# Performance work log

Measured on AMD Instinct MI355X. Metric: run time of the kernel, lower is better.

The kernel has to match this reference:

```python
import jax, jax.numpy as jnp
import numpy as np
from jax import lax

B, T, C = 32, 512, 128
K = 3                      # top_k periods
MIN_P, MAX_P = 8, 64       # period search band
P_MAX = MAX_P              # grid width
CYC_MAX = (T + MIN_P - 1) // MIN_P
KW = 9                     # cyc-axis depthwise kernel
GN_G = 32                  # _best_gn_groups(128)
EPS_GN = 1e-5
EPS_ORTH = 1e-6
EPS_W = 1e-8


def setup_inputs() -> dict:
    key = jax.random.key(0)
    ks = jax.random.split(key, 4)
    return {
        "x": jax.random.normal(ks[0], (B, T, C), jnp.float32),
        "W_dw": jax.random.normal(ks[1], (C, 1, KW), jnp.float32) * 0.1,
        "W_pw": jax.random.normal(ks[2], (C, C), jnp.float32) * (1.0 / np.sqrt(C)),
        "gn_weight": jnp.ones((C,), jnp.float32),
        "gn_bias": jnp.zeros((C,), jnp.float32),
        "W_gate": jax.random.normal(ks[3], (C, C), jnp.float32) * (1.0 / np.sqrt(C)),
        "gamma": jnp.full((C,), 1e-3, jnp.float32),
    }


def _autocorr_topk(x):
    # x: [B,T,C] -> period idx [B,K], softmax weights [B,K]
    Xf = jnp.fft.rfft(x, axis=1)
    Pm = (Xf * jnp.conj(Xf)).real.mean(-1)          # [B, T//2+1]
    r = jnp.fft.irfft(Pm, n=T, axis=1)              # [B, T] autocorrelation
    lag = jnp.arange(T)
    valid = (lag >= MIN_P) & (lag <= MAX_P)
    very_neg = jnp.finfo(x.dtype).min / 8
    rm = jnp.where(valid[None, :], r, very_neg)
    vals, idx = lax.top_k(rm, K)
    w = jax.nn.softmax(vals, axis=1)
    return idx, w


def _fold(s, p):
    # s: [N,T,C], p: [N] int periods -> Z [N,C,CYC_MAX,P_MAX], mask, unfold index maps
    N = s.shape[0]
    p = jnp.maximum(p, 1)
    tpad = ((T + p - 1) // p) * p                   # [N]
    cyc = jnp.arange(CYC_MAX)[None, :, None]
    pos = jnp.arange(P_MAX)[None, None, :]
    time = cyc * p[:, None, None] + pos             # [N,CYC_MAX,P_MAX]
    valid = (pos < p[:, None, None]) & (time < tpad[:, None, None])
    # right-side reflect padding indices
    m = 2 * (T - 1)
    rr = time % m
    src_idx = jnp.where(rr < T, rr, m - rr)
    src = jnp.take_along_axis(s, src_idx.reshape(N, -1)[:, :, None], axis=1)
    src = src.reshape(N, CYC_MAX, P_MAX, C) * valid[..., None].astype(s.dtype)
    Z = jnp.transpose(src, (0, 3, 1, 2))            # [N,C,CYC_MAX,P_MAX]
    mask2d = valid[:, None].astype(s.dtype)         # [N,1,CYC_MAX,P_MAX]
    t = jnp.arange(T)[None, :]
    cyc_T = jnp.clip(t // p[:, None], 0, CYC_MAX - 1)
    pos_T = jnp.clip(t % p[:, None], 0, P_MAX - 1)
    return Z, mask2d, cyc_T, pos_T


def _cyc_conv(Z, mask2d, W_dw, W_pw, gn_w, gn_b, W_gate, gamma):
    # CycAxisConv1d: mean over period axis, depthwise+pointwise conv along cyc,
    # GroupNorm, GELU, SE-gate, LayerScale residual broadcast back to 2D.
    N, _, L, _ = Z.shape
    u = Z.mean(-1)                                  # [N,C,L]
    h = lax.conv_general_dilated(u, W_dw, (1,), [(KW // 2, KW // 2)],
                                 dimension_numbers=('NCH', 'OIH', 'NCH'),
                                 feature_group_count=C)
    h = jnp.einsum('oc,ncl->nol', W_pw, h)
    hg = h.reshape(N, GN_G, C // GN_G, L)
    mean = hg.mean((2, 3), keepdims=True)
    var = hg.var((2, 3), keepdims=True)
    hg = (hg - mean) * lax.rsqrt(var + EPS_GN)
    h = hg.reshape(N, C, L) * gn_w[None, :, None] + gn_b[None, :, None]
    h = jax.nn.gelu(h, approximate=False)
    gate = jax.nn.sigmoid(jnp.einsum('oc,nc->no', W_gate, u.mean(-1)))
    h = h * gate[:, :, None]
    x2d = h[..., None] * gamma[None, :, None, None] * mask2d
    return Z + x2d


def _unfold(Z, cyc_T, pos_T):
    N = Z.shape[0]
    Zf = Z.reshape(N, C, CYC_MAX * P_MAX)
    sp = jnp.clip(cyc_T * P_MAX + pos_T, 0, CYC_MAX * P_MAX - 1)  # [N,T]
    y = jnp.take_along_axis(Zf, sp[:, None, :], axis=2)           # [N,C,T]
    return jnp.transpose(y, (0, 2, 1))                            # [N,T,C]


def reference(x, W_dw, W_pw, gn_weight, gn_bias, W_gate, gamma):
    idx, w = _autocorr_topk(x)                      # [B,K], [B,K]
    p_flat = idx.reshape(-1)                        # [B*K]
    s = jnp.repeat(x, K, axis=0)                    # [B*K,T,C]
    Z, mask2d, cyc_T, pos_T = _fold(s, p_flat)
    Z = _cyc_conv(Z, mask2d, W_dw, W_pw, gn_weight, gn_bias, W_gate, gamma)
    y = _unfold(Z, cyc_T, pos_T).reshape(B, K, T, C)
    periodic = jnp.einsum('bk,bktc->btc', w, y)
    # period confidence Gamma from weight entropy
    H = -(w * jnp.log(w + EPS_W)).sum(1)
    Gamma = jnp.clip(1.0 - H / (jnp.log(float(K) + EPS_W) + EPS_W), 0.0, 1.0)
    # orthogonal residual of local part against periodic part
    local = x - periodic
    num = (local * periodic).sum(1, keepdims=True)
    den = (periodic * periodic).sum(1, keepdims=True) + EPS_ORTH
    local_orth = local - num / den * periodic
    g = Gamma[:, None, None]
    return g * (periodic + local_orth) + (1.0 - g) * x
```

## Files before the change

### kernel.cpp

```cpp
#include <hip/hip_runtime.h>
#include <math.h>

static constexpr int Bn   = 32;
static constexpr int Tn   = 512;
static constexpr int Cn   = 128;
static constexpr int NLAG = 57;
static constexpr int CYC  = 64;

__global__ __launch_bounds__(256) void k_autocorr(const float* __restrict__ x,
    float* __restrict__ r_ws) {
  const int w   = (blockIdx.x & 7) * 32 + (blockIdx.x >> 3);
  const int b   = w >> 3;
  const int grp = w & 7;
  const int L0  = 8 + grp * 8;
  const int tid = threadIdx.x;
  const float4* X4 = (const float4*)(x + (size_t)b * Tn * Cn);

  float acc[8];
#pragma unroll
  for (int i = 0; i < 8; ++i) acc[i] = 0.f;

  for (int it = 0; it < 8; ++it) {
    const int id = it * 256 + tid;
    const int c4 = id & 31;
    const int t0 = (id >> 5) * 8;
    float4 A[8];
#pragma unroll
    for (int j = 0; j < 8; ++j) A[j] = X4[(t0 + j) * 32 + c4];
    float4 R[16];
#pragma unroll
    for (int j = 0; j < 16; ++j) R[j] = X4[((t0 + L0 + j) & 511) * 32 + c4];
#pragma unroll
    for (int g = 0; g < 8; ++g) {
#pragma unroll
      for (int j = 0; j < 8; ++j) {
        const float4 a = A[j];
        const float4 r = R[g + j];
        acc[g] += a.x * r.x + a.y * r.y + a.z * r.z + a.w * r.w;
      }
    }
  }

  __shared__ float lds_r[4][8];
  const int lane = tid & 63, wave = tid >> 6;
#pragma unroll
  for (int g = 0; g < 8; ++g) {
    float v = acc[g];
#pragma unroll
    for (int m = 32; m > 0; m >>= 1) v += __shfl_xor(v, m, 64);
    if (lane == 0) lds_r[wave][g] = v;
  }
  __syncthreads();
  if (tid < 8) {
    const int li = grp * 8 + tid;
    if (li < NLAG) {
      r_ws[b * NLAG + li] =
          (lds_r[0][tid] + lds_r[1][tid] + lds_r[2][tid] + lds_r[3][tid]) * (1.0f / Cn);
    }
  }
}

__global__ __launch_bounds__(512) void k_fold_conv(
    const float* __restrict__ x, const float* __restrict__ r_ws,
    const float* __restrict__ Wdw, const float* __restrict__ Wpw,
    const float* __restrict__ gnw, const float* __restrict__ gnb,
    const float* __restrict__ Wgate, float* __restrict__ hh) {
  const int n  = (blockIdx.x & 7) * 12 + (blockIdx.x >> 3);
  const int b  = n / 3, kk = n % 3;
  const int tid  = threadIdx.x;
  const int lane = tid & 63;
  const int wq   = __builtin_amdgcn_readfirstlane(tid >> 6);

  __shared__ float su[CYC * 129];
  __shared__ float sh[Cn * 65];
  __shared__ float ubar_s[Cn];
  __shared__ float gates_s[Cn];
  __shared__ int   p_sh;

  if (tid < 64) {
    const float* rb = r_ws + b * NLAG;
    float v  = (tid < NLAG) ? rb[tid] : -INFINITY;
    int  idx = tid;
    int  lag = 8;
#pragma unroll
    for (int k = 0; k < 3; ++k) {
      if (k > kk) break;
      float bv = v; int bi = idx;
#pragma unroll
      for (int m = 32; m > 0; m >>= 1) {
        const float ov = __shfl_xor(bv, m, 64);
        const int   oi = __shfl_xor(bi, m, 64);
        if (ov > bv || (ov == bv && oi < bi)) { bv = ov; bi = oi; }
      }
      lag = bi + 8;
      if (idx == bi) v = -INFINITY;
    }
    if (tid == 0) p_sh = lag;
  }
  __syncthreads();
  const int p    = p_sh;
  const int ncyc = (Tn + p - 1) / p;

  {
    const int l  = tid >> 3;
    const int c0 = (tid & 7) * 16;
    float a[16];
#pragma unroll
    for (int i = 0; i < 16; ++i) a[i] = 0.f;
    if (l < ncyc) {
      const float4* xb4 = (const float4*)(x + (size_t)b * Tn * Cn) + (c0 >> 2);
      const int base = l * p;
      for (int j = 0; j < p; ++j) {
        const int time = base + j;
        const int src  = time < Tn ? time : (2 * (Tn - 1) - time);
        const float4 v0 = xb4[src * 32 + 0];
        const float4 v1 = xb4[src * 32 + 1];
        const float4 v2 = xb4[src * 32 + 2];
        const float4 v3 = xb4[src * 32 + 3];
        a[0]  += v0.x; a[1]  += v0.y; a[2]  += v0.z; a[3]  += v0.w;
        a[4]  += v1.x; a[5]  += v1.y; a[6]  += v1.z; a[7]  += v1.w;
        a[8]  += v2.x; a[9]  += v2.y; a[10] += v2.z; a[11] += v2.w;
        a[12] += v3.x; a[13] += v3.y; a[14] += v3.z; a[15] += v3.w;
      }
    }
    float* dst = su + l * 129 + c0;
#pragma unroll
    for (int i = 0; i < 16; ++i) dst[i] = a[i] * (1.0f / 64.0f);
  }
  __syncthreads();

  if (tid < Cn) {
    float s = 0.f;
    for (int l = 0; l < CYC; ++l) s += su[l * 129 + tid];
    ubar_s[tid] = s * (1.0f / CYC);
  }

  {
    const int c0 = wq * 16;
#pragma unroll
    for (int i = 0; i < 16; ++i) {
      const int c = c0 + i;
      float s = 0.f;
#pragma unroll
      for (int k = 0; k < 9; ++k) {
        const int ll = lane + k - 4;
        if (ll >= 0 && ll < CYC) s += su[ll * 129 + c] * Wdw[c * 9 + k];
      }
      sh[c * 65 + lane] = s;
    }
  }
  __syncthreads();

  {
    const int ol   = lane & 15;
    const int part = lane >> 4;
    const int o    = wq * 16 + ol;
    float z = 0.f;
    const float* wg = Wgate + (size_t)o * Cn + part * 32;
    const float* ub = ubar_s + part * 32;
    for (int c = 0; c < 32; ++c) z += wg[c] * ub[c];
    z += __shfl_xor(z, 16, 64);
    z += __shfl_xor(z, 32, 64);
    if (part == 0) gates_s[o] = 1.0f / (1.0f + expf(-z));
  }

  float acc[16];
#pragma unroll
  for (int i = 0; i < 16; ++i) acc[i] = 0.f;
  const int o0 = wq * 16;
  {
    const float* wb = Wpw + (size_t)o0 * Cn;
    for (int c = 0; c < Cn; ++c) {
      const float hv = sh[c * 65 + lane];
#pragma unroll
      for (int i = 0; i < 16; ++i) acc[i] = fmaf(wb[i * Cn + c], hv, acc[i]);
    }
  }
  __syncthreads();

  float4 res[4];
#pragma unroll
  for (int g = 0; g < 4; ++g) {
    float s1 = acc[4*g] + acc[4*g+1] + acc[4*g+2] + acc[4*g+3];
    float s2 = acc[4*g]*acc[4*g] + acc[4*g+1]*acc[4*g+1]
             + acc[4*g+2]*acc[4*g+2] + acc[4*g+3]*acc[4*g+3];
#pragma unroll
    for (int m = 32; m > 0; m >>= 1) {
      s1 += __shfl_xor(s1, m, 64);
      s2 += __shfl_xor(s2, m, 64);
    }
    const float mean = s1 * (1.0f / 256.0f);
    const float var  = s2 * (1.0f / 256.0f) - mean * mean;
    const float rstd = rsqrtf(var + 1e-5f);
    float* rp = (float*)&res[g];
#pragma unroll
    for (int i = 0; i < 4; ++i) {
      const int o = o0 + 4*g + i;
      float h = (acc[4*g + i] - mean) * rstd;
      h = h * gnw[o] + gnb[o];
      h = 0.5f * h * (1.0f + erff(h * 0.70710678118654752440f));
      rp[i] = h * gates_s[o];
    }
  }
  float4* hp = (float4*)(hh + (size_t)n * CYC * Cn + (size_t)lane * Cn + o0);
#pragma unroll
  for (int g = 0; g < 4; ++g) hp[g] = res[g];
}

__global__ __launch_bounds__(128) void k_dot_out(
    const float* __restrict__ x, const float* __restrict__ hh,
    const float* __restrict__ r_ws, const float* __restrict__ gamma,
    float* __restrict__ out) {
  const int b  = blockIdx.x;
  const int cg = blockIdx.y;
  const int tid = threadIdx.x;
  const int c_l = tid & 15;
  const int tg  = tid >> 4;
  const int c   = cg * 16 + c_l;

  __shared__ float P_s[Tn * 16];
  __shared__ unsigned short cyc_s[Tn][3];
  __shared__ float params[4];
  __shared__ int   pp[3];
  __shared__ float red[2][2][16];
  __shared__ float sc_s[16];

  if (tid < 64) {
    const float* rb = r_ws + b * NLAG;
    float v  = (tid < NLAG) ? rb[tid] : -INFINITY;
    int  idx = tid;
    float vals[3]; int lags[3];
#pragma unroll
    for (int k = 0; k < 3; ++k) {
      float bv = v; int bi = idx;
#pragma unroll
      for (int m = 32; m > 0; m >>= 1) {
        const float ov = __shfl_xor(bv, m, 64);
        const int   oi = __shfl_xor(bi, m, 64);
        if (ov > bv || (ov == bv && oi < bi)) { bv = ov; bi = oi; }
      }
      vals[k] = bv; lags[k] = bi + 8;
      if (idx == bi) v = -INFINITY;
    }
    if (tid == 0) {
      const float m  = vals[0];
      const float e0 = expf(vals[0] - m), e1 = expf(vals[1] - m), e2 = expf(vals[2] - m);
      const float s  = e0 + e1 + e2;
      const float w0 = e0 / s, w1 = e1 / s, w2 = e2 / s;
      pp[0] = lags[0]; pp[1] = lags[1]; pp[2] = lags[2];
      params[0] = w0; params[1] = w1; params[2] = w2;
      const float H  = -(w0 * logf(w0 + 1e-8f) + w1 * logf(w1 + 1e-8f) + w2 * logf(w2 + 1e-8f));
      const float lg = logf(3.0f + 1e-8f) + 1e-8f;
      params[3] = fminf(fmaxf(1.0f - H / lg, 0.0f), 1.0f);
    }
  }
  __syncthreads();
  const int p0 = pp[0], p1 = pp[1], p2 = pp[2];
  const float w0 = params[0], w1 = params[1], w2 = params[2];
  const float g  = params[3];
  const float sw = w0 + w1 + w2;

  for (int t = tid; t < Tn; t += 128) {
    cyc_s[t][0] = (unsigned short)(t / p0);
    cyc_s[t][1] = (unsigned short)(t / p1);
    cyc_s[t][2] = (unsigned short)(t / p2);
  }
  __syncthreads();

  const float gam = gamma[c];
  const float* xb = x + (size_t)b * Tn * Cn;
  const float* h0 = hh + (size_t)(b * 3 + 0) * CYC * Cn + c;
  const float* h1 = hh + (size_t)(b * 3 + 1) * CYC * Cn + c;
  const float* h2 = hh + (size_t)(b * 3 + 2) * CYC * Cn + c;

  float na = 0.f, da = 0.f;
  for (int tt = 0; tt < 64; ++tt) {
    const int t = (tg << 6) + tt;
    const float xv = xb[t * Cn + c];
    const float dv = gam * (w0 * h0[cyc_s[t][0] * Cn] +
                            w1 * h1[cyc_s[t][1] * Cn] +
                            w2 * h2[cyc_s[t][2] * Cn]);
    const float P = sw * xv + dv;
    P_s[t * 16 + c_l] = P;
    na += (xv - P) * P;
    da += P * P;
  }
  na += __shfl_xor(na, 16, 64); da += __shfl_xor(da, 16, 64);
  na += __shfl_xor(na, 32, 64); da += __shfl_xor(da, 32, 64);
  const int wv_ = tid >> 6;
  if ((tid & 63) < 16) { red[0][wv_][c_l] = na; red[1][wv_][c_l] = da; }
  __syncthreads();
  if (tid < 16) {
    const float num = red[0][0][tid] + red[0][1][tid];
    const float den = red[1][0][tid] + red[1][1][tid] + 1e-6f;
    sc_s[tid] = g * (num / den);
  }
  __syncthreads();
  const float sc = sc_s[c_l];

  float* ob = out + (size_t)b * Tn * Cn;
  for (int tt = 0; tt < 64; ++tt) {
    const int t = (tg << 6) + tt;
    const float xv = xb[t * Cn + c];
    ob[t * Cn + c] = xv - sc * P_s[t * 16 + c_l];
  }
}

extern "C" void kernel_launch(void* const* d_in, const int* in_sizes, int n_in,
                              void* d_out, int out_size, void* d_ws, size_t ws_size,
                              hipStream_t stream) {
  const float* x     = (const float*)d_in[0];
  const float* Wdw   = (const float*)d_in[1];
  const float* Wpw   = (const float*)d_in[2];
  const float* gnw   = (const float*)d_in[3];
  const float* gnb   = (const float*)d_in[4];
  const float* Wgate = (const float*)d_in[5];
  const float* gamma = (const float*)d_in[6];
  float* out = (float*)d_out;

  char* ws = (char*)d_ws;
  float* r_ws = (float*)ws;
  float* hh   = (float*)(ws + 8192);

  k_autocorr<<<Bn * 8, 256, 0, stream>>>(x, r_ws);
  k_fold_conv<<<Bn * 3, 512, 0, stream>>>(x, r_ws, Wdw, Wpw, gnw, gnb, Wgate, hh);
  k_dot_out<<<dim3(Bn, 8), 128, 0, stream>>>(x, hh, r_ws, gamma, out);
}
```

Measured before the change: 150.7 us.

## Split fold and conv into separate kernels with finer-grained parallel grids

The single 96-block fold+conv kernel becomes two kernels. A 6144-block fold kernel computes per-cycle sums into a workspace buffer, and a 768-block conv kernel splits the output channels into 8 groups per sequence, with the gate computed per wave through shuffles. The output kernel moves to 256-thread blocks on a 1D remapped grid with interleaved time indexing. The aim is to fill the GPU's compute units instead of running 96 large blocks. The cost is an extra launch, a workspace round-trip, and the depthwise conv plus gate being recomputed in each of the 8 channel-group blocks.

```diff
diff --git a/kernel.cpp b/kernel.cpp
--- a/kernel.cpp
+++ b/kernel.cpp
@@ -6,6 +6,27 @@
 static constexpr int Cn   = 128;
 static constexpr int NLAG = 57;
 static constexpr int CYC  = 64;
+
+__device__ __forceinline__ int topk_p(const float* __restrict__ rb,
+                                      int tid, int kk) {
+  float v  = (tid < NLAG) ? rb[tid] : -INFINITY;
+  int  idx = tid;
+  int  lag = 8;
+#pragma unroll
+  for (int k = 0; k < 3; ++k) {
+    if (k > kk) break;
+    float bv = v; int bi = idx;
+#pragma unroll
+    for (int m = 32; m > 0; m >>= 1) {
+      const float ov = __shfl_xor(bv, m, 64);
+      const int   oi = __shfl_xor(bi, m, 64);
+      if (ov > bv || (ov == bv && oi < bi)) { bv = ov; bi = oi; }
+    }
+    lag = bi + 8;
+    if (idx == bi) v = -INFINITY;
+  }
+  return lag;
+}
 
 __global__ __launch_bounds__(256) void k_autocorr(const float* __restrict__ x,
     float* __restrict__ r_ws) {
@@ -60,159 +81,156 @@
   }
 }
 
-__global__ __launch_bounds__(512) void k_fold_conv(
-    const float* __restrict__ x, const float* __restrict__ r_ws,
-    const float* __restrict__ Wdw, const float* __restrict__ Wpw,
-    const float* __restrict__ gnw, const float* __restrict__ gnb,
-    const float* __restrict__ Wgate, float* __restrict__ hh) {
-  const int n  = (blockIdx.x & 7) * 12 + (blockIdx.x >> 3);
-  const int b  = n / 3, kk = n % 3;
-  const int tid  = threadIdx.x;
-  const int lane = tid & 63;
-  const int wq   = __builtin_amdgcn_readfirstlane(tid >> 6);
-
-  __shared__ float su[CYC * 129];
-  __shared__ float sh[Cn * 65];
-  __shared__ float ubar_s[Cn];
-  __shared__ float gates_s[Cn];
-  __shared__ int   p_sh;
-
+__global__ __launch_bounds__(128) void k_fold_u(const float* __restrict__ x,
+    const float* __restrict__ r_ws, float* __restrict__ u) {
+  const int bid = blockIdx.x;
+  const int w = (bid & 7) * 768 + (bid >> 3);
+  const int n = w >> 6, l = w & 63;
+  const int b = n / 3, kk = n % 3;
+  const int tid = threadIdx.x;
+
+  __shared__ int p_sh;
   if (tid < 64) {
-    const float* rb = r_ws + b * NLAG;
-    float v  = (tid < NLAG) ? rb[tid] : -INFINITY;
-    int  idx = tid;
-    int  lag = 8;
-#pragma unroll
-    for (int k = 0; k < 3; ++k) {
-      if (k > kk) break;
-      float bv = v; int bi = idx;
-#pragma unroll
-      for (int m = 32; m > 0; m >>= 1) {
-        const float ov = __shfl_xor(bv, m, 64);
-        const int   oi = __shfl_xor(bi, m, 64);
-        if (ov > bv || (ov == bv && oi < bi)) { bv = ov; bi = oi; }
-      }
-      lag = bi + 8;
-      if (idx == bi) v = -INFINITY;
-    }
+    const int lag = topk_p(r_ws + b * NLAG, tid, kk);
     if (tid == 0) p_sh = lag;
   }
   __syncthreads();
   const int p    = p_sh;
   const int ncyc = (Tn + p - 1) / p;
 
+  float acc = 0.f;
+  if (l < ncyc) {
+    const float* xb = x + (size_t)b * Tn * Cn;
+    const int base = l * p;
+    for (int j = 0; j < p; ++j) {
+      const int time = base + j;
+      const int src  = time < Tn ? time : (2 * (Tn - 1) - time);
+      acc += xb[src * Cn + tid];
+    }
+  }
+  u[((size_t)n * CYC + l) * Cn + tid] = acc * (1.0f / 64.0f);
+}
+
+__global__ __launch_bounds__(256) void k_conv(
+    const float* __restrict__ u, const float* __restrict__ Wdw,
+    const float* __restrict__ Wpw, const float* __restrict__ gnw,
+    const float* __restrict__ gnb, const float* __restrict__ Wgate,
+    float* __restrict__ hh) {
+  const int bid = blockIdx.x;
+  const int w = (bid & 7) * 96 + (bid >> 3);
+  const int n = w >> 3, og = w & 7;
+  const int tid  = threadIdx.x;
+  const int l    = tid & 63;
+  const int wq   = __builtin_amdgcn_readfirstlane(tid >> 6);
+
+  __shared__ float smem[8320];
+  __shared__ float ubar_s[Cn];
+
   {
-    const int l  = tid >> 3;
-    const int c0 = (tid & 7) * 16;
-    float a[16];
-#pragma unroll
-    for (int i = 0; i < 16; ++i) a[i] = 0.f;
-    if (l < ncyc) {
-      const float4* xb4 = (const float4*)(x + (size_t)b * Tn * Cn) + (c0 >> 2);
-      const int base = l * p;
-      for (int j = 0; j < p; ++j) {
-        const int time = base + j;
-        const int src  = time < Tn ? time : (2 * (Tn - 1) - time);
-        const float4 v0 = xb4[src * 32 + 0];
-        const float4 v1 = xb4[src * 32 + 1];
-        const float4 v2 = xb4[src * 32 + 2];
-        const float4 v3 = xb4[src * 32 + 3];
-        a[0]  += v0.x; a[1]  += v0.y; a[2]  += v0.z; a[3]  += v0.w;
-        a[4]  += v1.x; a[5]  += v1.y; a[6]  += v1.z; a[7]  += v1.w;
-        a[8]  += v2.x; a[9]  += v2.y; a[10] += v2.z; a[11] += v2.w;
-        a[12] += v3.x; a[13] += v3.y; a[14] += v3.z; a[15] += v3.w;
-      }
-    }
-    float* dst = su + l * 129 + c0;
-#pragma unroll
-    for (int i = 0; i < 16; ++i) dst[i] = a[i] * (1.0f / 64.0f);
+    const float4* u4 = (const float4*)(u + (size_t)n * CYC * Cn);
+#pragma unroll
+    for (int i = 0; i < 8; ++i) {
+      const int idx4 = i * 256 + tid;
+      const float4 v = u4[idx4];
+      const int ll = idx4 >> 5;
+      const int cc = (idx4 & 31) << 2;
+      float* d = smem + ll * 129 + cc;
+      d[0] = v.x; d[1] = v.y; d[2] = v.z; d[3] = v.w;
+    }
   }
   __syncthreads();
 
   if (tid < Cn) {
     float s = 0.f;
-    for (int l = 0; l < CYC; ++l) s += su[l * 129 + tid];
+    for (int ll = 0; ll < CYC; ++ll) s += smem[ll * 129 + tid];
     ubar_s[tid] = s * (1.0f / CYC);
   }
 
+  float hreg[32];
   {
-    const int c0 = wq * 16;
-#pragma unroll
-    for (int i = 0; i < 16; ++i) {
+    const int c0 = wq * 32;
+#pragma unroll
+    for (int i = 0; i < 32; ++i) {
       const int c = c0 + i;
       float s = 0.f;
 #pragma unroll
       for (int k = 0; k < 9; ++k) {
-        const int ll = lane + k - 4;
-        if (ll >= 0 && ll < CYC) s += su[ll * 129 + c] * Wdw[c * 9 + k];
+        const int ll = l + k - 4;
+        if (ll >= 0 && ll < CYC) s += smem[ll * 129 + c] * Wdw[c * 9 + k];
       }
-      sh[c * 65 + lane] = s;
-    }
-  }
-  __syncthreads();
-
+      hreg[i] = s;
+    }
+  }
+  __syncthreads();
+
+  float gi[4];
   {
-    const int ol   = lane & 15;
-    const int part = lane >> 4;
-    const int o    = wq * 16 + ol;
+    const int ol   = l & 3;
+    const int part = l >> 2;
+    const int o    = og * 16 + wq * 4 + ol;
     float z = 0.f;
-    const float* wg = Wgate + (size_t)o * Cn + part * 32;
-    const float* ub = ubar_s + part * 32;
-    for (int c = 0; c < 32; ++c) z += wg[c] * ub[c];
+    const float* wg = Wgate + (size_t)o * Cn + part * 8;
+    const float* ub = ubar_s + part * 8;
+#pragma unroll
+    for (int cc = 0; cc < 8; ++cc) z += wg[cc] * ub[cc];
+    z += __shfl_xor(z, 4, 64);
+    z += __shfl_xor(z, 8, 64);
     z += __shfl_xor(z, 16, 64);
     z += __shfl_xor(z, 32, 64);
-    if (part == 0) gates_s[o] = 1.0f / (1.0f + expf(-z));
-  }
-
-  float acc[16];
-#pragma unroll
-  for (int i = 0; i < 16; ++i) acc[i] = 0.f;
-  const int o0 = wq * 16;
+    const float sig = 1.0f / (1.0f + expf(-z));
+#pragma unroll
+    for (int i = 0; i < 4; ++i) gi[i] = __shfl(sig, i, 64);
+  }
+
   {
-    const float* wb = Wpw + (size_t)o0 * Cn;
-    for (int c = 0; c < Cn; ++c) {
-      const float hv = sh[c * 65 + lane];
-#pragma unroll
-      for (int i = 0; i < 16; ++i) acc[i] = fmaf(wb[i * Cn + c], hv, acc[i]);
-    }
-  }
-  __syncthreads();
-
-  float4 res[4];
-#pragma unroll
-  for (int g = 0; g < 4; ++g) {
-    float s1 = acc[4*g] + acc[4*g+1] + acc[4*g+2] + acc[4*g+3];
-    float s2 = acc[4*g]*acc[4*g] + acc[4*g+1]*acc[4*g+1]
-             + acc[4*g+2]*acc[4*g+2] + acc[4*g+3]*acc[4*g+3];
-#pragma unroll
-    for (int m = 32; m > 0; m >>= 1) {
-      s1 += __shfl_xor(s1, m, 64);
-      s2 += __shfl_xor(s2, m, 64);
-    }
-    const float mean = s1 * (1.0f / 256.0f);
-    const float var  = s2 * (1.0f / 256.0f) - mean * mean;
-    const float rstd = rsqrtf(var + 1e-5f);
-    float* rp = (float*)&res[g];
-#pragma unroll
-    for (int i = 0; i < 4; ++i) {
-      const int o = o0 + 4*g + i;
-      float h = (acc[4*g + i] - mean) * rstd;
-      h = h * gnw[o] + gnb[o];
-      h = 0.5f * h * (1.0f + erff(h * 0.70710678118654752440f));
-      rp[i] = h * gates_s[o];
-    }
-  }
-  float4* hp = (float4*)(hh + (size_t)n * CYC * Cn + (size_t)lane * Cn + o0);
-#pragma unroll
-  for (int g = 0; g < 4; ++g) hp[g] = res[g];
-}
-
-__global__ __launch_bounds__(128) void k_dot_out(
+    const int c0 = wq * 32;
+#pragma unroll
+    for (int i = 0; i < 32; ++i) smem[(c0 + i) * 65 + l] = hreg[i];
+  }
+  __syncthreads();
+
+  const int o4 = og * 16 + wq * 4;
+  float acc[4];
+#pragma unroll
+  for (int i = 0; i < 4; ++i) acc[i] = 0.f;
+  const float* wb = Wpw + (size_t)o4 * Cn;
+  for (int c = 0; c < Cn; ++c) {
+    const float hv = smem[c * 65 + l];
+#pragma unroll
+    for (int i = 0; i < 4; ++i) acc[i] = fmaf(wb[i * Cn + c], hv, acc[i]);
+  }
+
+  float s1 = acc[0] + acc[1] + acc[2] + acc[3];
+  float s2 = acc[0]*acc[0] + acc[1]*acc[1] + acc[2]*acc[2] + acc[3]*acc[3];
+#pragma unroll
+  for (int m = 32; m > 0; m >>= 1) {
+    s1 += __shfl_xor(s1, m, 64);
+    s2 += __shfl_xor(s2, m, 64);
+  }
+  const float mean = s1 * (1.0f / 256.0f);
+  const float var  = s2 * (1.0f / 256.0f) - mean * mean;
+  const float rstd = rsqrtf(var + 1e-5f);
+
+  float4 res;
+  float* rp = (float*)&res;
+#pragma unroll
+  for (int i = 0; i < 4; ++i) {
+    const int o = o4 + i;
+    float h = (acc[i] - mean) * rstd;
+    h = h * gnw[o] + gnb[o];
+    h = 0.5f * h * (1.0f + erff(h * 0.70710678118654752440f));
+    rp[i] = h * gi[i];
+  }
+  *(float4*)(hh + (size_t)n * CYC * Cn + (size_t)l * Cn + o4) = res;
+}
+
+__global__ __launch_bounds__(256) void k_dot_out(
     const float* __restrict__ x, const float* __restrict__ hh,
     const float* __restrict__ r_ws, const float* __restrict__ gamma,
     float* __restrict__ out) {
-  const int b  = blockIdx.x;
-  const int cg = blockIdx.y;
+  const int bid = blockIdx.x;
+  const int w = (bid & 7) * 32 + (bid >> 3);
+  const int b = w >> 3, cg = w & 7;
   const int tid = threadIdx.x;
   const int c_l = tid & 15;
   const int tg  = tid >> 4;
@@ -222,7 +240,7 @@
   __shared__ unsigned short cyc_s[Tn][3];
   __shared__ float params[4];
   __shared__ int   pp[3];
-  __shared__ float red[2][2][16];
+  __shared__ float red[2][4][16];
   __shared__ float sc_s[16];
 
   if (tid < 64) {
@@ -260,7 +278,7 @@
   const float g  = params[3];
   const float sw = w0 + w1 + w2;
 
-  for (int t = tid; t < Tn; t += 128) {
+  for (int t = tid; t < Tn; t += 256) {
     cyc_s[t][0] = (unsigned short)(t / p0);
     cyc_s[t][1] = (unsigned short)(t / p1);
     cyc_s[t][2] = (unsigned short)(t / p2);
@@ -274,8 +292,9 @@
   const float* h2 = hh + (size_t)(b * 3 + 2) * CYC * Cn + c;
 
   float na = 0.f, da = 0.f;
-  for (int tt = 0; tt < 64; ++tt) {
-    const int t = (tg << 6) + tt;
+#pragma unroll 4
+  for (int tt = 0; tt < 32; ++tt) {
+    const int t = tt * 16 + tg;
     const float xv = xb[t * Cn + c];
     const float dv = gam * (w0 * h0[cyc_s[t][0] * Cn] +
                             w1 * h1[cyc_s[t][1] * Cn] +
@@ -291,16 +310,17 @@
   if ((tid & 63) < 16) { red[0][wv_][c_l] = na; red[1][wv_][c_l] = da; }
   __syncthreads();
   if (tid < 16) {
-    const float num = red[0][0][tid] + red[0][1][tid];
-    const float den = red[1][0][tid] + red[1][1][tid] + 1e-6f;
+    const float num = red[0][0][tid] + red[0][1][tid] + red[0][2][tid] + red[0][3][tid];
+    const float den = red[1][0][tid] + red[1][1][tid] + red[1][2][tid] + red[1][3][tid] + 1e-6f;
     sc_s[tid] = g * (num / den);
   }
   __syncthreads();
   const float sc = sc_s[c_l];
 
   float* ob = out + (size_t)b * Tn * Cn;
-  for (int tt = 0; tt < 64; ++tt) {
-    const int t = (tg << 6) + tt;
+#pragma unroll 4
+  for (int tt = 0; tt < 32; ++tt) {
+    const int t = tt * 16 + tg;
     const float xv = xb[t * Cn + c];
     ob[t * Cn + c] = xv - sc * P_s[t * 16 + c_l];
   }
@@ -320,9 +340,11 @@
 
   char* ws = (char*)d_ws;
   float* r_ws = (float*)ws;
-  float* hh   = (float*)(ws + 8192);
+  float* u    = (float*)(ws + 8192);
+  float* hh   = (float*)(ws + 8192 + 3145728);
 
   k_autocorr<<<Bn * 8, 256, 0, stream>>>(x, r_ws);
-  k_fold_conv<<<Bn * 3, 512, 0, stream>>>(x, r_ws, Wdw, Wpw, gnw, gnb, Wgate, hh);
-  k_dot_out<<<dim3(Bn, 8), 128, 0, stream>>>(x, hh, r_ws, gamma, out);
-}
+  k_fold_u<<<6144, 128, 0, stream>>>(x, r_ws, u);
+  k_conv<<<768, 256, 0, stream>>>(u, Wdw, Wpw, gnw, gnb, Wgate, hh);
+  k_dot_out<<<256, 256, 0, stream>>>(x, hh, r_ws, gamma, out);
+}
```

New measurement: 138.9 us. 1.09x faster.
